# Optimization experiments

Measured on AMD Instinct MI355X. Metric: run time of the kernel, lower is better.

The kernel has to match this reference:

```python
import jax, jax.numpy as jnp
import numpy as np

N_NODES = 100000
D_FEAT = 128
N_EDGES = 300000
HIDDEN = 64


def setup_inputs() -> dict:
    key = jax.random.key(0)
    k1, k2, k3, k4 = jax.random.split(key, 4)
    node_emb = jax.random.normal(k1, (N_NODES, D_FEAT), dtype=jnp.float32)
    train_sample = jax.random.randint(k2, (N_EDGES, 2), 0, N_NODES, dtype=jnp.int64)
    input_dim = 2 * D_FEAT
    r1 = np.sqrt(6.0 / input_dim)
    w1 = jax.random.uniform(k3, (input_dim, HIDDEN), minval=-r1, maxval=r1, dtype=jnp.float32)
    b1 = jnp.zeros((HIDDEN,), dtype=jnp.float32)
    r2 = np.sqrt(6.0 / HIDDEN)
    w2 = jax.random.uniform(k4, (HIDDEN, 1), minval=-r2, maxval=r2, dtype=jnp.float32)
    return {"input": node_emb, "train_sample": train_sample, "w1": w1, "b1": b1, "w2": w2}


def reference(input, train_sample, w1, b1, w2):
    # gather source/target node embeddings: [E, D] each
    src = input[train_sample[:, 0]]
    dst = input[train_sample[:, 1]]
    h = jnp.concatenate([src, dst], axis=1)  # [E, 2D]
    x = jax.nn.relu(h @ w1 + b1)             # [E, HIDDEN]
    return x @ w2                             # [E, 1]
```

## Files before the change

kernel.cpp:

```cpp
#include <hip/hip_runtime.h>
#include <hip/hip_bf16.h>


#define D_FEAT 128
#define HIDDEN 64

typedef __attribute__((ext_vector_type(8))) short v8s;
typedef __attribute__((ext_vector_type(4))) float f32x4;

__device__ inline unsigned short f2bf(float f) {
    return __builtin_bit_cast(unsigned short, __float2bfloat16(f));
}

__device__ inline bool detect_is64(const int* ts32, int lane) {
    int probe = ts32[2 * lane + 1];
    return __ballot(probe != 0) == 0ULL;
}

__global__ void __launch_bounds__(256)
precompute_kernel(const float* __restrict__ emb, const float* __restrict__ w1,
                  const float* __restrict__ b1, unsigned short* __restrict__ P,
                  int n_nodes) {
    __shared__ unsigned short bt[16384];
    const int t    = threadIdx.x;
    const int lane = t & 63;
    const int wid  = t >> 6;
    const int sub  = lane & 15;
    const int g    = lane >> 4;

    {
        const int k    = t & 127;
        const int half = t >> 7;
        const float4* src = reinterpret_cast<const float4*>(w1 + (size_t)t * 64);
#pragma unroll
        for (int j4 = 0; j4 < 16; ++j4) {
            const float4 v = src[j4];
            const int cb = half * 64 + j4 * 4;
            bt[((cb + 0) * 128 + k) ^ (((cb + 0) & 7) << 3)] = f2bf(v.x);
            bt[((cb + 1) * 128 + k) ^ (((cb + 1) & 7) << 3)] = f2bf(v.y);
            bt[((cb + 2) * 128 + k) ^ (((cb + 2) & 7) << 3)] = f2bf(v.z);
            bt[((cb + 3) * 128 + k) ^ (((cb + 3) & 7) << 3)] = f2bf(v.w);
        }
    }

    float4 bias[4];
#pragma unroll
    for (int nj = 0; nj < 4; ++nj)
        bias[nj] = *reinterpret_cast<const float4*>(b1 + nj * 16 + g * 4);

    __syncthreads();

    const int ntiles = (n_nodes + 15) / 16;
    const int gwave  = blockIdx.x * 4 + wid;
    const int nwave  = gridDim.x * 4;

    auto loadA = [&](float4* a, int tt) {
        int row = tt * 16 + sub;
        if (row >= n_nodes) row = n_nodes - 1;
        const float* p = emb + (size_t)row * D_FEAT + g * 8;
#pragma unroll
        for (int ks = 0; ks < 4; ++ks) {
            a[2 * ks]     = *reinterpret_cast<const float4*>(p + ks * 32);
            a[2 * ks + 1] = *reinterpret_cast<const float4*>(p + ks * 32 + 4);
        }
    };

    float4 A0[8], A1[8];
    if (gwave < ntiles) loadA(A0, gwave);

    for (int tt = gwave; tt < ntiles; tt += nwave) {
        const int tn = tt + nwave;
        if (tn < ntiles) loadA(A1, tn);

        f32x4 acc[8];
#pragma unroll
        for (int nj = 0; nj < 8; ++nj) acc[nj] = (f32x4){0.f, 0.f, 0.f, 0.f};

#pragma unroll
        for (int ks = 0; ks < 4; ++ks) {
            const int k0 = ks * 32;
            const float4 a0 = A0[2 * ks], a1 = A0[2 * ks + 1];
            v8s af;
            af[0] = (short)f2bf(a0.x); af[1] = (short)f2bf(a0.y);
            af[2] = (short)f2bf(a0.z); af[3] = (short)f2bf(a0.w);
            af[4] = (short)f2bf(a1.x); af[5] = (short)f2bf(a1.y);
            af[6] = (short)f2bf(a1.z); af[7] = (short)f2bf(a1.w);
#pragma unroll
            for (int nj = 0; nj < 8; ++nj) {
                const int c = nj * 16 + sub;
                const int eidx = (c * 128 + k0 + g * 8) ^ ((c & 7) << 3);
                const v8s bf = *reinterpret_cast<const v8s*>(&bt[eidx]);
                acc[nj] = __builtin_amdgcn_mfma_f32_16x16x32_bf16(bf, af, acc[nj], 0, 0, 0);
            }
        }

        const int node = tt * 16 + sub;
        if (node < n_nodes) {
#pragma unroll
            for (int nj = 0; nj < 8; ++nj) {
                float b0 = 0.f, b1v = 0.f, b2 = 0.f, b3 = 0.f;
                if (nj < 4) { b0 = bias[nj].x; b1v = bias[nj].y;
                              b2 = bias[nj].z; b3 = bias[nj].w; }
                ushort4 o;
                o.x = f2bf(acc[nj][0] + b0);
                o.y = f2bf(acc[nj][1] + b1v);
                o.z = f2bf(acc[nj][2] + b2);
                o.w = f2bf(acc[nj][3] + b3);
                *reinterpret_cast<ushort4*>(P + (size_t)node * 128 + nj * 16 + g * 4) = o;
            }
        }

#pragma unroll
        for (int i = 0; i < 8; ++i) A0[i] = A1[i];
    }
}

__device__ inline float pairterm(unsigned aw, unsigned bw, float w0, float w1) {
    float a0 = __builtin_bit_cast(float, aw << 16);
    float a1 = __builtin_bit_cast(float, aw & 0xFFFF0000u);
    float b0 = __builtin_bit_cast(float, bw << 16);
    float b1 = __builtin_bit_cast(float, bw & 0xFFFF0000u);
    float h0 = a0 + b0; h0 = h0 > 0.f ? h0 : 0.f;
    float h1 = a1 + b1; h1 = h1 > 0.f ? h1 : 0.f;
    return h0 * w0 + h1 * w1;
}

__global__ void __launch_bounds__(256)
edge_kernel(const unsigned short* __restrict__ P, const void* __restrict__ ts,
            const float* __restrict__ w2, float* __restrict__ out, int n_edges) {
    const int lane = threadIdx.x & 63;
    const int wid  = threadIdx.x >> 6;
    const int sub  = lane & 7;
    const int grp  = lane >> 3;
    const int gw   = blockIdx.x * 4 + wid;
    const int nw   = gridDim.x * 4;

    const int* ts32 = (const int*)ts;
    const long long* ts64 = (const long long*)ts;
    const bool is64 = detect_is64(ts32, lane);

    const float4 w2a = *reinterpret_cast<const float4*>(w2 + sub * 8);
    const float4 w2b = *reinterpret_cast<const float4*>(w2 + sub * 8 + 4);

    for (int e = gw * 8 + grp; e < n_edges; e += nw * 8) {
        long long s, d;
        if (is64) { s = ts64[2 * e]; d = ts64[2 * e + 1]; }
        else      { s = ts32[2 * e]; d = ts32[2 * e + 1]; }
        const uint4 a = *reinterpret_cast<const uint4*>(P + (size_t)s * 128 + sub * 8);
        const uint4 b = *reinterpret_cast<const uint4*>(P + (size_t)d * 128 + 64 + sub * 8);
        float v = pairterm(a.x, b.x, w2a.x, w2a.y)
                + pairterm(a.y, b.y, w2a.z, w2a.w)
                + pairterm(a.z, b.z, w2b.x, w2b.y)
                + pairterm(a.w, b.w, w2b.z, w2b.w);
#pragma unroll
        for (int off = 1; off < 8; off <<= 1) v += __shfl_xor(v, off);
        if (sub == 0) out[e] = v;
    }
}

__global__ void __launch_bounds__(256)
direct_kernel(const float* __restrict__ emb, const void* __restrict__ ts,
              const float* __restrict__ w1, const float* __restrict__ b1,
              const float* __restrict__ w2, float* __restrict__ out, int n_edges) {
    const int lane = threadIdx.x & 63;
    const int gw   = blockIdx.x * (blockDim.x >> 6) + (threadIdx.x >> 6);
    const int nw   = gridDim.x * (blockDim.x >> 6);
    const float w2v  = w2[lane];
    const float bias = b1[lane];
    const int* ts32 = (const int*)ts;
    const long long* ts64 = (const long long*)ts;
    const bool is64 = detect_is64(ts32, lane);

    for (int e = gw; e < n_edges; e += nw) {
        long long s, d;
        if (is64) { s = ts64[2 * e]; d = ts64[2 * e + 1]; }
        else      { s = ts32[2 * e]; d = ts32[2 * e + 1]; }
        const float4* s4 = reinterpret_cast<const float4*>(emb + s * D_FEAT);
        const float4* d4 = reinterpret_cast<const float4*>(emb + d * D_FEAT);
        float acc = bias;
#pragma unroll
        for (int k4 = 0; k4 < 32; ++k4) {
            float4 r = s4[k4];
            acc += r.x * w1[(4 * k4 + 0) * 64 + lane];
            acc += r.y * w1[(4 * k4 + 1) * 64 + lane];
            acc += r.z * w1[(4 * k4 + 2) * 64 + lane];
            acc += r.w * w1[(4 * k4 + 3) * 64 + lane];
        }
#pragma unroll
        for (int k4 = 0; k4 < 32; ++k4) {
            float4 r = d4[k4];
            acc += r.x * w1[(128 + 4 * k4 + 0) * 64 + lane];
            acc += r.y * w1[(128 + 4 * k4 + 1) * 64 + lane];
            acc += r.z * w1[(128 + 4 * k4 + 2) * 64 + lane];
            acc += r.w * w1[(128 + 4 * k4 + 3) * 64 + lane];
        }
        float h = acc > 0.0f ? acc : 0.0f;
        float v = h * w2v;
#pragma unroll
        for (int off = 32; off > 0; off >>= 1) v += __shfl_xor(v, off);
        if (lane == 0) out[e] = v;
    }
}

extern "C" void kernel_launch(void* const* d_in, const int* in_sizes, int n_in,
                              void* d_out, int out_size, void* d_ws, size_t ws_size,
                              hipStream_t stream) {
    const float* emb = (const float*)d_in[0];
    const void*  ts  = d_in[1];
    const float* w1  = (const float*)d_in[2];
    const float* b1  = (const float*)d_in[3];
    const float* w2  = (const float*)d_in[4];
    float* out = (float*)d_out;

    const int n_nodes = in_sizes[0] / D_FEAT;
    const int n_edges = in_sizes[1] / 2;

    const size_t p_bytes = (size_t)n_nodes * 128 * sizeof(unsigned short);

    if (ws_size >= p_bytes) {
        unsigned short* P = (unsigned short*)d_ws;
        precompute_kernel<<<782, 256, 0, stream>>>(emb, w1, b1, P, n_nodes);
        edge_kernel<<<2048, 256, 0, stream>>>(P, ts, w2, out, n_edges);
    } else {
        direct_kernel<<<2048, 256, 0, stream>>>(emb, ts, w1, b1, w2, out, n_edges);
    }
}
```

Measured before the change: 44.67 us.

## Hoist B fragments into registers, cheaper bf16 packing, retune precompute grid

The precompute kernel now loads all W1 bf16 fragments from LDS into registers once per wave instead of re-reading LDS for every tile. The float-to-bf16 conversion becomes a biased-add round plus a byte-permute pack instead of the library conversion. Launch bounds allow two blocks per CU and the grid drops from 782 to 512 blocks. This cuts LDS traffic and conversion ALU work but raises register pressure (32 v8s fragments). It also changes rounding: half-up instead of round-to-nearest-even, with no NaN handling.

After: 37.53 us. 16.0% less time.

```diff
diff --git a/kernel.cpp b/kernel.cpp
--- a/kernel.cpp
+++ b/kernel.cpp
@@ -7,9 +7,16 @@
 
 typedef __attribute__((ext_vector_type(8))) short v8s;
 typedef __attribute__((ext_vector_type(4))) float f32x4;
-
-__device__ inline unsigned short f2bf(float f) {
-    return __builtin_bit_cast(unsigned short, __float2bfloat16(f));
+typedef __attribute__((ext_vector_type(4))) unsigned u32x4;
+
+__device__ inline unsigned short f2bf_rn(float f) {
+    unsigned u = __builtin_bit_cast(unsigned, f) + 0x8000u;
+    return (unsigned short)(u >> 16);
+}
+__device__ inline unsigned pack2(float lo, float hi) {
+    unsigned ul = __builtin_bit_cast(unsigned, lo) + 0x8000u;
+    unsigned uh = __builtin_bit_cast(unsigned, hi) + 0x8000u;
+    return __builtin_amdgcn_perm(uh, ul, 0x07060302u);
 }
 
 __device__ inline bool detect_is64(const int* ts32, int lane) {
@@ -17,7 +24,7 @@
     return __ballot(probe != 0) == 0ULL;
 }
 
-__global__ void __launch_bounds__(256)
+__global__ void __launch_bounds__(256, 2)
 precompute_kernel(const float* __restrict__ emb, const float* __restrict__ w1,
                   const float* __restrict__ b1, unsigned short* __restrict__ P,
                   int n_nodes) {
@@ -36,10 +43,10 @@
         for (int j4 = 0; j4 < 16; ++j4) {
             const float4 v = src[j4];
             const int cb = half * 64 + j4 * 4;
-            bt[((cb + 0) * 128 + k) ^ (((cb + 0) & 7) << 3)] = f2bf(v.x);
-            bt[((cb + 1) * 128 + k) ^ (((cb + 1) & 7) << 3)] = f2bf(v.y);
-            bt[((cb + 2) * 128 + k) ^ (((cb + 2) & 7) << 3)] = f2bf(v.z);
-            bt[((cb + 3) * 128 + k) ^ (((cb + 3) & 7) << 3)] = f2bf(v.w);
+            bt[((cb + 0) * 128 + k) ^ (((cb + 0) & 7) << 3)] = f2bf_rn(v.x);
+            bt[((cb + 1) * 128 + k) ^ (((cb + 1) & 7) << 3)] = f2bf_rn(v.y);
+            bt[((cb + 2) * 128 + k) ^ (((cb + 2) & 7) << 3)] = f2bf_rn(v.z);
+            bt[((cb + 3) * 128 + k) ^ (((cb + 3) & 7) << 3)] = f2bf_rn(v.w);
         }
     }
 
@@ -49,6 +56,16 @@
         bias[nj] = *reinterpret_cast<const float4*>(b1 + nj * 16 + g * 4);
 
     __syncthreads();
+
+    v8s B[4][8];
+#pragma unroll
+    for (int ks = 0; ks < 4; ++ks)
+#pragma unroll
+        for (int nj = 0; nj < 8; ++nj) {
+            const int c = nj * 16 + sub;
+            const int eidx = (c * 128 + ks * 32 + g * 8) ^ ((c & 7) << 3);
+            B[ks][nj] = *reinterpret_cast<const v8s*>(&bt[eidx]);
+        }
 
     const int ntiles = (n_nodes + 15) / 16;
     const int gwave  = blockIdx.x * 4 + wid;
@@ -71,42 +88,38 @@
     for (int tt = gwave; tt < ntiles; tt += nwave) {
         const int tn = tt + nwave;
         if (tn < ntiles) loadA(A1, tn);
-
         f32x4 acc[8];
 #pragma unroll
         for (int nj = 0; nj < 8; ++nj) acc[nj] = (f32x4){0.f, 0.f, 0.f, 0.f};
 
 #pragma unroll
         for (int ks = 0; ks < 4; ++ks) {
-            const int k0 = ks * 32;
             const float4 a0 = A0[2 * ks], a1 = A0[2 * ks + 1];
-            v8s af;
-            af[0] = (short)f2bf(a0.x); af[1] = (short)f2bf(a0.y);
-            af[2] = (short)f2bf(a0.z); af[3] = (short)f2bf(a0.w);
-            af[4] = (short)f2bf(a1.x); af[5] = (short)f2bf(a1.y);
-            af[6] = (short)f2bf(a1.z); af[7] = (short)f2bf(a1.w);
-#pragma unroll
-            for (int nj = 0; nj < 8; ++nj) {
-                const int c = nj * 16 + sub;
-                const int eidx = (c * 128 + k0 + g * 8) ^ ((c & 7) << 3);
-                const v8s bf = *reinterpret_cast<const v8s*>(&bt[eidx]);
-                acc[nj] = __builtin_amdgcn_mfma_f32_16x16x32_bf16(bf, af, acc[nj], 0, 0, 0);
-            }
+            u32x4 ap;
+            ap[0] = pack2(a0.x, a0.y);
+            ap[1] = pack2(a0.z, a0.w);
+            ap[2] = pack2(a1.x, a1.y);
+            ap[3] = pack2(a1.z, a1.w);
+            const v8s af = __builtin_bit_cast(v8s, ap);
+#pragma unroll
+            for (int nj = 0; nj < 8; ++nj)
+                acc[nj] = __builtin_amdgcn_mfma_f32_16x16x32_bf16(B[ks][nj], af,
+                                                                  acc[nj], 0, 0, 0);
         }
 
         const int node = tt * 16 + sub;
         if (node < n_nodes) {
+            unsigned short* prow = P + (size_t)node * 128;
 #pragma unroll
             for (int nj = 0; nj < 8; ++nj) {
-                float b0 = 0.f, b1v = 0.f, b2 = 0.f, b3 = 0.f;
-                if (nj < 4) { b0 = bias[nj].x; b1v = bias[nj].y;
-                              b2 = bias[nj].z; b3 = bias[nj].w; }
-                ushort4 o;
-                o.x = f2bf(acc[nj][0] + b0);
-                o.y = f2bf(acc[nj][1] + b1v);
-                o.z = f2bf(acc[nj][2] + b2);
-                o.w = f2bf(acc[nj][3] + b3);
-                *reinterpret_cast<ushort4*>(P + (size_t)node * 128 + nj * 16 + g * 4) = o;
+                float s0 = acc[nj][0], s1 = acc[nj][1];
+                float s2 = acc[nj][2], s3 = acc[nj][3];
+                if (nj < 4) { s0 += bias[nj].x; s1 += bias[nj].y;
+                              s2 += bias[nj].z; s3 += bias[nj].w; }
+                uint2 o;
+                o.x = pack2(s0, s1);
+                o.y = pack2(s2, s3);
+                *reinterpret_cast<uint2*>(prow + nj * 16 + g * 4) = o;
             }
         }
 
@@ -219,7 +232,7 @@
 
     if (ws_size >= p_bytes) {
         unsigned short* P = (unsigned short*)d_ws;
-        precompute_kernel<<<782, 256, 0, stream>>>(emb, w1, b1, P, n_nodes);
+        precompute_kernel<<<512, 256, 0, stream>>>(emb, w1, b1, P, n_nodes);
         edge_kernel<<<2048, 256, 0, stream>>>(P, ts, w2, out, n_edges);
     } else {
         direct_kernel<<<2048, 256, 0, stream>>>(emb, ts, w1, b1, w2, out, n_edges);
```
